# Optimization experiments

Hardware: AMD Instinct MI355X
Metric: run time of the kernel (lower is better)

The kernel has to match this reference:

```python
import jax, jax.numpy as jnp
import numpy as np

N, F, E, C, CELL = 2048, 64, 4, 3, 15
OUT_CH, OUT_K, N_CLASS = 10, 15, 2


def _xex(X, A_attr, wx0, wx1, we):
    # pairwise score tensor: Y[i,j] = X[i]@wx0 + X[j]@wx1 + A_attr[i,j]@we -> [N,N,c_out]
    return (X @ wx0)[:, None, :] + (X @ wx1)[None, :, :] + jnp.einsum('ije,ec->ijc', A_attr, we)


def _gcn_layer(X, A, A_attr, ax0, ax1, ae, ix0, ix1, ie, gx0, gx1, ge, wr):
    n = X.shape[0]
    # multi-channel attention (MA) branch
    att = jax.nn.elu(_xex(X, A_attr, ax0, ax1, ae)) + 1.0001  # [n,n,C]
    att = att * A[:, :, None]
    att = jax.nn.softmax(att, axis=1)  # softmax over neighbor axis (incl. zeroed entries, as in TF code)
    att = att * A[:, :, None]
    y_node = jnp.einsum('ijc,jf->icf', att, X).reshape(n, -1)        # [n, C*F_in]
    y_edge = jnp.einsum('ijc,ije->ice', att, A_attr).reshape(n, -1)  # [n, C*E]
    # gated branch (unmasked sum over all j, as in aggr_neibors_gate)
    info = jnp.tanh(_xex(X, A_attr, ix0, ix1, ie))        # [n,n,CELL]
    gate = jax.nn.sigmoid(_xex(X, A_attr, gx0, gx1, ge))  # [n,n,CELL]
    y_gate = jnp.sum(info * gate, axis=1)                 # [n, CELL]
    r = jnp.concatenate([X, y_edge, y_node, y_gate], axis=1)
    return jnp.tanh(r @ wr + 0.1)


def _forward(X, A, A_attr,
             att0_x0, att0_x1, att0_e, info0_x0, info0_x1, info0_e,
             gate0_x0, gate0_x1, gate0_e, r0,
             att1_x0, att1_x1, att1_e, info1_x0, info1_x1, info1_e,
             gate1_x0, gate1_x1, gate1_e, r1,
             out_att, out_cnn, out_r):
    h0 = _gcn_layer(X, A, A_attr, att0_x0, att0_x1, att0_e,
                    info0_x0, info0_x1, info0_e, gate0_x0, gate0_x1, gate0_e, r0)
    h1 = _gcn_layer(h0, A, A_attr, att1_x0, att1_x1, att1_e,
                    info1_x0, info1_x1, info1_e, gate1_x0, gate1_x1, gate1_e, r1)
    Xc = jnp.concatenate([X, h0, h1], axis=1)       # [n, F + 2*CELL]
    att = jax.nn.softmax(Xc @ out_att, axis=0)      # node-wise attention pooling, [n, OUT_CH]
    image = att.T @ Xc                              # [OUT_CH, F + 2*CELL]
    image = jnp.tanh(image @ out_cnn + 0.1)         # [OUT_CH, OUT_K]
    logits = image.reshape(1, -1) @ out_r + 0.1
    return jax.nn.softmax(logits, axis=-1)          # [1, N_CLASS]


def setup_inputs() -> dict:
    keys = jax.random.split(jax.random.key(0), 26)
    tn = lambda k, s: jax.random.normal(k, s, jnp.float32) * 0.05  # truncated_normal init approx
    return {
        'X': jax.random.normal(keys[0], (N, F), jnp.float32),
        'A': (jax.random.uniform(keys[1], (N, N)) < 0.02).astype(jnp.float32),  # ~40 neighbors/node
        'A_attr': jax.random.normal(keys[2], (N, N, E), jnp.float32),
        'att0_x0': tn(keys[3], (F, C)), 'att0_x1': tn(keys[4], (F, C)), 'att0_e': tn(keys[5], (E, C)),
        'info0_x0': tn(keys[6], (F, CELL)), 'info0_x1': tn(keys[7], (F, CELL)), 'info0_e': tn(keys[8], (E, CELL)),
        'gate0_x0': tn(keys[9], (F, CELL)), 'gate0_x1': tn(keys[10], (F, CELL)), 'gate0_e': tn(keys[11], (E, CELL)),
        'r0': tn(keys[12], (F + (F + E) * C + CELL, CELL)),
        'att1_x0': tn(keys[13], (CELL, C)), 'att1_x1': tn(keys[14], (CELL, C)), 'att1_e': tn(keys[15], (E, C)),
        'info1_x0': tn(keys[16], (CELL, CELL)), 'info1_x1': tn(keys[17], (CELL, CELL)), 'info1_e': tn(keys[18], (E, CELL)),
        'gate1_x0': tn(keys[19], (CELL, CELL)), 'gate1_x1': tn(keys[20], (CELL, CELL)), 'gate1_e': tn(keys[21], (E, CELL)),
        'r1': tn(keys[22], (CELL + (CELL + E) * C + CELL, CELL)),
        'out_att': tn(keys[23], (F + 2 * CELL, OUT_CH)),
        'out_cnn': tn(keys[24], (F + 2 * CELL, OUT_K)),
        'out_r': tn(keys[25], (OUT_K * OUT_CH, N_CLASS)),
    }


def reference(X, A, A_attr,
              att0_x0, att0_x1, att0_e, info0_x0, info0_x1, info0_e,
              gate0_x0, gate0_x1, gate0_e, r0,
              att1_x0, att1_x1, att1_e, info1_x0, info1_x1, info1_e,
              gate1_x0, gate1_x1, gate1_e, r1,
              out_att, out_cnn, out_r):
    return _forward(X, A, A_attr,
                    att0_x0, att0_x1, att0_e, info0_x0, info0_x1, info0_e,
                    gate0_x0, gate0_x1, gate0_e, r0,
                    att1_x0, att1_x1, att1_e, info1_x0, info1_x1, info1_e,
                    gate1_x0, gate1_x1, gate1_e, r1,
                    out_att, out_cnn, out_r)
```

## Files before the change

kernel.cpp:

```cpp
#include <hip/hip_runtime.h>
#include <hip/hip_bf16.h>
#include <math.h>

#define NN 2048
#define EE 4
#define CC 3
#define CELL 15
#define MAXD 128
#define GATE_JZ 4

typedef unsigned short u16;
typedef float f32x2 __attribute__((ext_vector_type(2)));

__device__ __forceinline__ float b2f(u16 u) { return __uint_as_float(((unsigned int)u) << 16); }
__device__ __forceinline__ u16 f2b(float f) {
    unsigned int x = __float_as_uint(f);
    unsigned int r = (x + 0x7fffu + ((x >> 16) & 1u)) >> 16;
    return (u16)r;
}
__device__ __forceinline__ float fastrcp(float x) { return __builtin_amdgcn_rcpf(x); }
__device__ __forceinline__ float fastexp2(float x) { return __builtin_amdgcn_exp2f(x); }
__device__ __forceinline__ float rfl(float x) {
    return __uint_as_float(__builtin_amdgcn_readfirstlane(__float_as_uint(x)));
}
__device__ __forceinline__ float ldx(const void* p, size_t i, bool bf) {
    if (bf) return b2f(((const u16*)p)[i]);
    return ((const float*)p)[i];
}
__device__ __forceinline__ bool detect_bf(const u16* X) {
    int lane = threadIdx.x & 63;
    u16 u = X[2 * lane];
    int e = (u >> 7) & 0xFF;
    unsigned long long m = __ballot(e >= 100 && e <= 150);
    return __popcll(m) >= 32;
}

__global__ __launch_bounds__(256) void k_edges(const void* __restrict__ A, const u16* __restrict__ Xd,
                                               int* __restrict__ flag, int* __restrict__ deg,
                                               int* __restrict__ edges) {
    bool bf = detect_bf(Xd);
    if (blockIdx.x == 0 && threadIdx.x == 0) *flag = bf ? 1 : 0;
    int lane = threadIdx.x & 63, wv = threadIdx.x >> 6;
    int i = blockIdx.x * 4 + wv;
    int base = 0;
    for (int jb = 0; jb < NN; jb += 64) {
        float a = ldx(A, (size_t)i * NN + jb + lane, bf);
        unsigned long long m = __ballot(a != 0.f);
        if (a != 0.f) {
            int slot = base + __popcll(m & ((1ull << lane) - 1ull));
            if (slot < MAXD) edges[i * MAXD + slot] = jb + lane;
        }
        base += __popcll(m);
    }
    if (lane == 0) deg[i] = base;
}

template<int FIN, bool XRAW>
__global__ void k_proj(const int* __restrict__ flag, const void* __restrict__ Xin_,
                       const void* __restrict__ ax0, const void* __restrict__ ax1,
                       const void* __restrict__ ix0, const void* __restrict__ ix1,
                       const void* __restrict__ gx0, const void* __restrict__ gx1,
                       float* __restrict__ p0, float* __restrict__ pj,
                       float* __restrict__ pa0, float* __restrict__ pa1) {
    __shared__ float xs[FIN];
    bool bf = (*flag != 0);
    bool xbf = XRAW ? bf : false;
    int nd = blockIdx.x;
    int t = threadIdx.x;
    if (t < FIN) xs[t] = ldx(Xin_, (size_t)nd * FIN + t, xbf);
    __syncthreads();
    if (t >= 66) return;
    const void* W; int col, OUT; float* dst;
    if (t < 15)      { W = ix0; col = t;      OUT = CELL; dst = p0  + nd * 30 + t; }
    else if (t < 30) { W = gx0; col = t - 15; OUT = CELL; dst = p0  + nd * 30 + t; }
    else if (t < 45) { W = ix1; col = t - 30; OUT = CELL; dst = pj  + nd * 30 + (t - 30); }
    else if (t < 60) { W = gx1; col = t - 45; OUT = CELL; dst = pj  + nd * 30 + (t - 30); }
    else if (t < 63) { W = ax0; col = t - 60; OUT = CC;   dst = pa0 + nd * 3 + (t - 60); }
    else             { W = ax1; col = t - 63; OUT = CC;   dst = pa1 + nd * 3 + (t - 63); }
    float acc = 0.f;
    for (int f = 0; f < FIN; ++f) acc += xs[f] * ldx(W, (size_t)f * OUT + col, bf);
    *dst = acc;
}

template<int FIN, bool BF, bool XRAW>
__device__ void att_body(const void* __restrict__ Xin_, const void* __restrict__ A_attr,
                         const void* __restrict__ ae,
                         const float* __restrict__ pa0, const float* __restrict__ pa1,
                         const int* __restrict__ deg, const int* __restrict__ edges,
                         float* __restrict__ y_node, float* __restrict__ y_edge,
                         float (*ew)[4], float* pdn, float* pne, float* pnn) {
    int i = blockIdx.x;
    int t = threadIdx.x;
    int lane = t & 63, wv = t >> 6;
    float aew[EE][CC];
    #pragma unroll
    for (int e = 0; e < EE; ++e)
        #pragma unroll
        for (int c = 0; c < CC; ++c) aew[e][c] = ldx(ae, e * CC + c, BF);
    float pa0v[3] = { pa0[i*3], pa0[i*3+1], pa0[i*3+2] };
    int dg = deg[i]; if (dg > MAXD) dg = MAXD;
    float dn[3] = {0.f, 0.f, 0.f};
    float ne[3][4] = {{0.f}};
    for (int base = 0; base < dg; base += 256) {
        int idx = base + t;
        if (idx < dg) {
            int j = edges[i * MAXD + idx];
            float a0, a1, a2, a3;
            if (BF) {
                const u16* ap = (const u16*)A_attr + ((size_t)i * NN + j) * EE;
                ushort4 av = *(const ushort4*)ap;
                a0 = b2f(av.x); a1 = b2f(av.y); a2 = b2f(av.z); a3 = b2f(av.w);
            } else {
                const float* ap = (const float*)A_attr + ((size_t)i * NN + j) * EE;
                float4 av = *(const float4*)ap;
                a0 = av.x; a1 = av.y; a2 = av.z; a3 = av.w;
            }
            float w[3];
            #pragma unroll
            for (int c = 0; c < 3; ++c) {
                float s = pa0v[c] + pa1[j*3 + c]
                        + a0*aew[0][c] + a1*aew[1][c] + a2*aew[2][c] + a3*aew[3][c];
                float val = (s > 0.f) ? (s + 1.0001f) : (__expf(s) - 1.f + 1.0001f);
                float wc = __expf(val);
                w[c] = wc;
                dn[c] += wc;
                ne[c][0] += wc * a0; ne[c][1] += wc * a1; ne[c][2] += wc * a2; ne[c][3] += wc * a3;
            }
            ew[idx][0] = __int_as_float(j);
            ew[idx][1] = w[0]; ew[idx][2] = w[1]; ew[idx][3] = w[2];
        }
    }
    #pragma unroll
    for (int off = 32; off; off >>= 1) {
        #pragma unroll
        for (int c = 0; c < 3; ++c) {
            dn[c] += __shfl_xor(dn[c], off);
            #pragma unroll
            for (int e = 0; e < 4; ++e) ne[c][e] += __shfl_xor(ne[c][e], off);
        }
    }
    if (lane == 0) {
        #pragma unroll
        for (int c = 0; c < 3; ++c) {
            pdn[wv*3 + c] = dn[c];
            #pragma unroll
            for (int e = 0; e < 4; ++e) pne[(wv*3 + c)*4 + e] = ne[c][e];
        }
    }
    __syncthreads();
    float rdn[3];
    #pragma unroll
    for (int c = 0; c < 3; ++c) {
        float s = (float)(NN - dg);
        #pragma unroll
        for (int w2 = 0; w2 < 4; ++w2) s += pdn[w2*3 + c];
        rdn[c] = 1.f / s;
    }
    float nn0 = 0.f, nn1 = 0.f, nn2 = 0.f;
    bool xbf = XRAW ? BF : false;
    for (int idx = wv; idx < dg; idx += 4) {
        int j = __float_as_int(ew[idx][0]);
        float w0 = ew[idx][1], w1 = ew[idx][2], w2 = ew[idx][3];
        if (lane < FIN) {
            float x = ldx(Xin_, (size_t)j * FIN + lane, xbf);
            nn0 += w0 * x; nn1 += w1 * x; nn2 += w2 * x;
        }
    }
    if (lane < FIN) {
        pnn[(wv*3 + 0)*64 + lane] = nn0;
        pnn[(wv*3 + 1)*64 + lane] = nn1;
        pnn[(wv*3 + 2)*64 + lane] = nn2;
    }
    __syncthreads();
    if (t < FIN) {
        #pragma unroll
        for (int c = 0; c < 3; ++c) {
            float s = pnn[(0*3+c)*64 + t] + pnn[(1*3+c)*64 + t]
                    + pnn[(2*3+c)*64 + t] + pnn[(3*3+c)*64 + t];
            y_node[(size_t)i * (3*FIN) + c*FIN + t] = s * rdn[c];
        }
    }
    if (t == 0) {
        #pragma unroll
        for (int c = 0; c < 3; ++c)
            #pragma unroll
            for (int e = 0; e < 4; ++e) {
                float s = pne[(0*3+c)*4+e] + pne[(1*3+c)*4+e] + pne[(2*3+c)*4+e] + pne[(3*3+c)*4+e];
                y_edge[(size_t)i * 12 + c*4 + e] = s * rdn[c];
            }
    }
}

template<int FIN, bool XRAW>
__global__ __launch_bounds__(256) void k_att(
        const int* __restrict__ flag,
        const void* __restrict__ Xin_, const void* __restrict__ A_attr, const void* __restrict__ ae,
        const float* __restrict__ pa0, const float* __restrict__ pa1,
        const int* __restrict__ deg, const int* __restrict__ edges,
        float* __restrict__ y_node, float* __restrict__ y_edge) {
    __shared__ float ew[MAXD][4];
    __shared__ float pdn[4*3];
    __shared__ float pne[4*3*4];
    __shared__ float pnn[4*3*64];
    if (*flag) att_body<FIN, true,  XRAW>(Xin_, A_attr, ae, pa0, pa1, deg, edges, y_node, y_edge, ew, pdn, pne, pnn);
    else       att_body<FIN, false, XRAW>(Xin_, A_attr, ae, pa0, pa1, deg, edges, y_node, y_edge, ew, pdn, pne, pnn);
}

template<bool BF, int K0, int NK>
__device__ void gate_half(const void* __restrict__ A_attr,
                          const void* __restrict__ iew, const void* __restrict__ gew,
                          const float* __restrict__ p0, const float* __restrict__ pj,
                          float* __restrict__ ygp, float* lds) {
    constexpr int T = 128;
    constexpr int JCH = NN / GATE_JZ;
    constexpr float L2E = 1.4426950408889634f;
    const int lane = threadIdx.x & 63;
    const int i = blockIdx.x * 4 + (threadIdx.x >> 6);
    const int jb0 = blockIdx.z * JCH;

    f32x2 W2[EE][NK];
    #pragma unroll
    for (int e = 0; e < EE; ++e)
        #pragma unroll
        for (int k = 0; k < NK; ++k) {
            W2[e][k].x = rfl(ldx(iew, e*CELL + K0 + k, BF) * (-2.f * L2E));
            W2[e][k].y = rfl(ldx(gew, e*CELL + K0 + k, BF) * (-L2E));
        }
    f32x2 p0p[NK];
    #pragma unroll
    for (int k = 0; k < NK; ++k) {
        p0p[k].x = rfl(p0[(size_t)i*30 + K0 + k] * (-2.f * L2E));
        p0p[k].y = rfl(p0[(size_t)i*30 + 15 + K0 + k] * (-L2E));
    }
    float acc[NK] = {0.f};

    for (int tb = jb0; tb < jb0 + JCH; tb += T) {
        __syncthreads();
        #pragma unroll
        for (int s = 0; s < 8; ++s) {
            int q = threadIdx.x + 256 * s;
            int r = q >> 4, c = q & 15;
            if (c < 2 * NK) {
                int k = c >> 1, comp = c & 1;
                float scale = comp ? (-L2E) : (-2.f * L2E);
                int ksrc = comp ? (15 + K0 + k) : (K0 + k);
                lds[r * 18 + c] = pj[(size_t)(tb + r) * 30 + ksrc] * scale;
            }
        }
        __syncthreads();
        #pragma unroll
        for (int js = 0; js < T; js += 64) {
            int r = js + lane;
            int j = tb + r;
            float a0, a1, a2, a3;
            if (BF) {
                const u16* ap = (const u16*)A_attr + ((size_t)i * NN + j) * EE;
                ushort4 av = *(const ushort4*)ap;
                a0 = b2f(av.x); a1 = b2f(av.y); a2 = b2f(av.z); a3 = b2f(av.w);
            } else {
                const float* ap = (const float*)A_attr + ((size_t)i * NN + j) * EE;
                float4 av = *(const float4*)ap;
                a0 = av.x; a1 = av.y; a2 = av.z; a3 = av.w;
            }
            f32x2 aa0 = {a0, a0}, aa1 = {a1, a1}, aa2 = {a2, a2}, aa3 = {a3, a3};
            const float* rowp = lds + r * 18;
            #pragma unroll
            for (int k = 0; k < NK; ++k) {
                f32x2 tu = *(const f32x2*)(rowp + 2*k) + p0p[k];
                tu += aa0 * W2[0][k];
                tu += aa1 * W2[1][k];
                tu += aa2 * W2[2][k];
                tu += aa3 * W2[3][k];
                float e1 = fastexp2(tu.x);
                float e2 = fastexp2(tu.y);
                float d1 = 1.f + e1, d2 = 1.f + e2;
                acc[k] = fmaf(1.f - e1, fastrcp(d1 * d2), acc[k]);
            }
        }
    }
    #pragma unroll
    for (int off = 32; off; off >>= 1)
        #pragma unroll
        for (int k = 0; k < NK; ++k) acc[k] += __shfl_xor(acc[k], off);
    if (lane == 0) {
        #pragma unroll
        for (int k = 0; k < NK; ++k)
            ygp[((size_t)blockIdx.z * NN + i) * CELL + K0 + k] = acc[k];
    }
}

__global__ __launch_bounds__(256, 2) void k_gate(
        const int* __restrict__ flag,
        const void* __restrict__ A_attr, const void* __restrict__ iew, const void* __restrict__ gew,
        const float* __restrict__ p0, const float* __restrict__ pj, float* __restrict__ ygp) {
    __shared__ __align__(16) float lds[128 * 18];
    if (*flag) {
        if (blockIdx.y == 0) gate_half<true, 0, 8>(A_attr, iew, gew, p0, pj, ygp, lds);
        else                 gate_half<true, 8, 7>(A_attr, iew, gew, p0, pj, ygp, lds);
    } else {
        if (blockIdx.y == 0) gate_half<false, 0, 8>(A_attr, iew, gew, p0, pj, ygp, lds);
        else                 gate_half<false, 8, 7>(A_attr, iew, gew, p0, pj, ygp, lds);
    }
}

__global__ __launch_bounds__(256) void k_hp(const int* __restrict__ flag,
        const void* __restrict__ X, const float* __restrict__ y_edge,
        const float* __restrict__ y_node, const float* __restrict__ y_gate,
        const void* __restrict__ wr,
        const void* __restrict__ ax0, const void* __restrict__ ax1,
        const void* __restrict__ ix0, const void* __restrict__ ix1,
        const void* __restrict__ gx0, const void* __restrict__ gx1,
        float* __restrict__ h0,
        float* __restrict__ p0o, float* __restrict__ pjo,
        float* __restrict__ pa0o, float* __restrict__ pa1o) {
    __shared__ float v[283];
    __shared__ float part[CELL][16];
    __shared__ float hs[CELL];
    bool bf = (*flag != 0);
    int nd = blockIdx.x, t = threadIdx.x;
    for (int q = t; q < 64; q += 256)  v[q]       = ldx(X, (size_t)nd * 64 + q, bf);
    for (int q = t; q < 12; q += 256)  v[64 + q]  = y_edge[(size_t)nd * 12 + q];
    for (int q = t; q < 192; q += 256) v[76 + q]  = y_node[(size_t)nd * 192 + q];
    for (int q = t; q < 15; q += 256) {
        float s = 0.f;
        #pragma unroll
        for (int z = 0; z < GATE_JZ; ++z) s += y_gate[((size_t)z * NN + nd) * CELL + q];
        v[268 + q] = s;
    }
    __syncthreads();
    if (t < 240) {
        int k = t >> 4, sub = t & 15;
        float acc = 0.f;
        for (int r = sub; r < 283; r += 16) acc += v[r] * ldx(wr, (size_t)r * CELL + k, bf);
        part[k][sub] = acc;
    }
    __syncthreads();
    if (t < CELL) {
        float acc = 0.1f;
        #pragma unroll
        for (int s = 0; s < 16; ++s) acc += part[t][s];
        float hv = tanhf(acc);
        hs[t] = hv;
        h0[(size_t)nd * CELL + t] = hv;
    }
    __syncthreads();
    if (t < 66) {
        const void* W; int col, OUT; float* dst;
        if (t < 15)      { W = ix0; col = t;      OUT = CELL; dst = p0o  + nd * 30 + t; }
        else if (t < 30) { W = gx0; col = t - 15; OUT = CELL; dst = p0o  + nd * 30 + t; }
        else if (t < 45) { W = ix1; col = t - 30; OUT = CELL; dst = pjo  + nd * 30 + (t - 30); }
        else if (t < 60) { W = gx1; col = t - 45; OUT = CELL; dst = pjo  + nd * 30 + (t - 30); }
        else if (t < 63) { W = ax0; col = t - 60; OUT = CC;   dst = pa0o + nd * 3 + (t - 60); }
        else             { W = ax1; col = t - 63; OUT = CC;   dst = pa1o + nd * 3 + (t - 63); }
        float acc = 0.f;
        for (int f = 0; f < CELL; ++f) acc += hs[f] * ldx(W, (size_t)f * OUT + col, bf);
        *dst = acc;
    }
}

__global__ __launch_bounds__(256) void k_hf(const int* __restrict__ flag,
        const void* __restrict__ X, const float* __restrict__ h0,
        const float* __restrict__ y_edge, const float* __restrict__ y_node,
        const float* __restrict__ y_gate, const void* __restrict__ wr,
        const void* __restrict__ oatt,
        float* __restrict__ h1, float* __restrict__ P) {
    __shared__ float v[87];
    __shared__ float xv[64];
    __shared__ float part[CELL][16];
    __shared__ float hs[CELL];
    __shared__ float pp[10][16];
    bool bf = (*flag != 0);
    int nd = blockIdx.x, t = threadIdx.x;
    for (int q = t; q < 15; q += 256) v[q]      = h0[(size_t)nd * 15 + q];
    for (int q = t; q < 12; q += 256) v[15 + q] = y_edge[(size_t)nd * 12 + q];
    for (int q = t; q < 45; q += 256) v[27 + q] = y_node[(size_t)nd * 45 + q];
    for (int q = t; q < 15; q += 256) {
        float s = 0.f;
        #pragma unroll
        for (int z = 0; z < GATE_JZ; ++z) s += y_gate[((size_t)z * NN + nd) * CELL + q];
        v[72 + q] = s;
    }
    for (int q = t; q < 64; q += 256) xv[q]     = ldx(X, (size_t)nd * 64 + q, bf);
    __syncthreads();
    if (t < 240) {
        int k = t >> 4, sub = t & 15;
        float acc = 0.f;
        for (int r = sub; r < 87; r += 16) acc += v[r] * ldx(wr, (size_t)r * CELL + k, bf);
        part[k][sub] = acc;
    }
    __syncthreads();
    if (t < CELL) {
        float acc = 0.1f;
        #pragma unroll
        for (int s = 0; s < 16; ++s) acc += part[t][s];
        float hv = tanhf(acc);
        hs[t] = hv;
        h1[(size_t)nd * CELL + t] = hv;
    }
    __syncthreads();
    if (t < 160) {
        int c = t >> 4, sub = t & 15;
        float acc = 0.f;
        for (int d = sub; d < 94; d += 16) {
            float x = (d < 64) ? xv[d] : (d < 79) ? v[d - 64] : hs[d - 79];
            acc += x * ldx(oatt, (size_t)d * 10 + c, bf);
        }
        pp[c][sub] = acc;
    }
    __syncthreads();
    if (t < 10) {
        float acc = 0.f;
        #pragma unroll
        for (int s = 0; s < 16; ++s) acc += pp[t][s];
        P[(size_t)nd * 10 + t] = acc;
    }
}

__global__ __launch_bounds__(1024) void k_f2(const float* __restrict__ P, float* __restrict__ wsm,
                                             float* __restrict__ imgp) {
    __shared__ float red[16][10];
    int t = threadIdx.x; int lane = t & 63; int wv = t >> 6;
    for (int q = t; q < 940; q += 1024) imgp[q] = 0.f;
    float mx[10], sm[10];
    #pragma unroll
    for (int c = 0; c < 10; ++c) mx[c] = -1e30f;
    for (int n = t; n < NN; n += 1024)
        #pragma unroll
        for (int c = 0; c < 10; ++c) mx[c] = fmaxf(mx[c], P[(size_t)n*10 + c]);
    #pragma unroll
    for (int off = 32; off; off >>= 1)
        #pragma unroll
        for (int c = 0; c < 10; ++c) mx[c] = fmaxf(mx[c], __shfl_xor(mx[c], off));
    if (lane == 0)
        #pragma unroll
        for (int c = 0; c < 10; ++c) red[wv][c] = mx[c];
    __syncthreads();
    #pragma unroll
    for (int c = 0; c < 10; ++c) {
        float m = red[0][c];
        for (int w2 = 1; w2 < 16; ++w2) m = fmaxf(m, red[w2][c]);
        mx[c] = m;
    }
    __syncthreads();
    #pragma unroll
    for (int c = 0; c < 10; ++c) sm[c] = 0.f;
    for (int n = t; n < NN; n += 1024)
        #pragma unroll
        for (int c = 0; c < 10; ++c) sm[c] += __expf(P[(size_t)n*10 + c] - mx[c]);
    #pragma unroll
    for (int off = 32; off; off >>= 1)
        #pragma unroll
        for (int c = 0; c < 10; ++c) sm[c] += __shfl_xor(sm[c], off);
    if (lane == 0)
        #pragma unroll
        for (int c = 0; c < 10; ++c) red[wv][c] = sm[c];
    __syncthreads();
    float rs[10];
    #pragma unroll
    for (int c = 0; c < 10; ++c) {
        float s = 0.f;
        for (int w2 = 0; w2 < 16; ++w2) s += red[w2][c];
        rs[c] = 1.f / s;
    }
    for (int n = t; n < NN; n += 1024)
        #pragma unroll
        for (int c = 0; c < 10; ++c) wsm[(size_t)n*10 + c] = __expf(P[(size_t)n*10 + c] - mx[c]) * rs[c];
}

__global__ __launch_bounds__(1024) void k_f3(const int* __restrict__ flag,
                     const void* __restrict__ X, const float* __restrict__ h0,
                     const float* __restrict__ h1, const float* __restrict__ wsm,
                     float* __restrict__ image_pre) {
    bool bf = (*flag != 0);
    int t = threadIdx.x;
    if (t >= 940) return;
    int ch = t / 94, d = t - ch * 94;
    int n0 = blockIdx.x * 32;
    float acc = 0.f;
    for (int nl = 0; nl < 32; ++nl) {
        int n = n0 + nl;
        float w = wsm[(size_t)n*10 + ch];
        float x = (d < 64) ? ldx(X, (size_t)n*64 + d, bf)
                : (d < 79) ? h0[(size_t)n*15 + (d - 64)]
                           : h1[(size_t)n*15 + (d - 79)];
        acc += w * x;
    }
    atomicAdd(&image_pre[t], acc);
}

__global__ __launch_bounds__(256) void k_f4(const int* __restrict__ flag,
                     const float* __restrict__ image_pre,
                     const void* __restrict__ out_cnn, const void* __restrict__ out_r,
                     void* __restrict__ out) {
    bool bf = (*flag != 0);
    __shared__ float ip[940];
    __shared__ float img2[150];
    __shared__ float red[8];
    int t = threadIdx.x;
    for (int q = t; q < 940; q += 256) ip[q] = image_pre[q];
    __syncthreads();
    if (t < 150) {
        int ch = t / 15, kk = t - ch * 15;
        float acc = 0.1f;
        for (int d = 0; d < 94; ++d) acc += ip[ch*94 + d] * ldx(out_cnn, (size_t)d*15 + kk, bf);
        img2[t] = tanhf(acc);
    }
    __syncthreads();
    float c0 = 0.f, c1 = 0.f;
    if (t < 150) {
        float vv = img2[t];
        c0 = vv * ldx(out_r, (size_t)t*2, bf);
        c1 = vv * ldx(out_r, (size_t)t*2 + 1, bf);
    }
    #pragma unroll
    for (int off = 32; off; off >>= 1) { c0 += __shfl_xor(c0, off); c1 += __shfl_xor(c1, off); }
    if ((t & 63) == 0) { red[(t >> 6)*2] = c0; red[(t >> 6)*2 + 1] = c1; }
    __syncthreads();
    if (t == 0) {
        float l0 = 0.1f + red[0] + red[2] + red[4] + red[6];
        float l1 = 0.1f + red[1] + red[3] + red[5] + red[7];
        float m = fmaxf(l0, l1);
        float e0 = __expf(l0 - m), e1 = __expf(l1 - m);
        float s = e0 + e1;
        float p0v = e0 / s, p1v = e1 / s;
        if (bf) { u16* o = (u16*)out; o[0] = f2b(p0v); o[1] = f2b(p1v); }
        else    { float* o = (float*)out; o[0] = p0v; o[1] = p1v; }
    }
}

extern "C" void kernel_launch(void* const* d_in, const int* in_sizes, int n_in,
                              void* d_out, int out_size, void* d_ws, size_t ws_size,
                              hipStream_t stream) {
    (void)in_sizes; (void)n_in; (void)out_size; (void)ws_size;
    const void* X      = d_in[0];
    const void* A      = d_in[1];
    const void* Aattr  = d_in[2];
    const void* a0x0 = d_in[3],  *a0x1 = d_in[4],  *a0e = d_in[5];
    const void* i0x0 = d_in[6],  *i0x1 = d_in[7],  *i0e = d_in[8];
    const void* g0x0 = d_in[9],  *g0x1 = d_in[10], *g0e = d_in[11];
    const void* r0   = d_in[12];
    const void* a1x0 = d_in[13], *a1x1 = d_in[14], *a1e = d_in[15];
    const void* i1x0 = d_in[16], *i1x1 = d_in[17], *i1e = d_in[18];
    const void* g1x0 = d_in[19], *g1x1 = d_in[20], *g1e = d_in[21];
    const void* r1   = d_in[22];
    const void* oatt = d_in[23], *ocnn = d_in[24], *orr = d_in[25];

    char* p = (char*)d_ws;
    auto alloc = [&](size_t bytes) -> void* { void* r = (void*)p; p += (bytes + 255) & ~(size_t)255; return r; };
    int*   flag   = (int*)  alloc(4);
    int*   deg    = (int*)  alloc(NN * 4);
    int*   edges  = (int*)  alloc((size_t)NN * MAXD * 4);
    float* p0_0   = (float*)alloc((size_t)NN * 30 * 4);
    float* pj_0   = (float*)alloc((size_t)NN * 30 * 4);
    float* pa0_0  = (float*)alloc((size_t)NN * 3 * 4);
    float* pa1_0  = (float*)alloc((size_t)NN * 3 * 4);
    float* p0_1   = (float*)alloc((size_t)NN * 30 * 4);
    float* pj_1   = (float*)alloc((size_t)NN * 30 * 4);
    float* pa0_1  = (float*)alloc((size_t)NN * 3 * 4);
    float* pa1_1  = (float*)alloc((size_t)NN * 3 * 4);
    float* ye0    = (float*)alloc((size_t)NN * 12 * 4);
    float* yn0    = (float*)alloc((size_t)NN * 192 * 4);
    float* yg0    = (float*)alloc((size_t)GATE_JZ * NN * CELL * 4);
    float* h0     = (float*)alloc((size_t)NN * CELL * 4);
    float* ye1    = (float*)alloc((size_t)NN * 12 * 4);
    float* yn1    = (float*)alloc((size_t)NN * 45 * 4);
    float* yg1    = (float*)alloc((size_t)GATE_JZ * NN * CELL * 4);
    float* h1     = (float*)alloc((size_t)NN * CELL * 4);
    float* P      = (float*)alloc((size_t)NN * 10 * 4);
    float* wsm    = (float*)alloc((size_t)NN * 10 * 4);
    float* imgp   = (float*)alloc(940 * 4);

    k_edges<<<NN / 4, 256, 0, stream>>>(A, (const u16*)X, flag, deg, edges);

    dim3 ggate(NN / 4, 2, GATE_JZ);

    k_proj<64, true><<<NN, 128, 0, stream>>>(flag, X, a0x0, a0x1, i0x0, i0x1, g0x0, g0x1, p0_0, pj_0, pa0_0, pa1_0);
    k_att<64, true><<<NN, 256, 0, stream>>>(flag, X, Aattr, a0e, pa0_0, pa1_0, deg, edges, yn0, ye0);
    k_gate<<<ggate, 256, 0, stream>>>(flag, Aattr, i0e, g0e, p0_0, pj_0, yg0);
    k_hp<<<NN, 256, 0, stream>>>(flag, X, ye0, yn0, yg0, r0,
                                 a1x0, a1x1, i1x0, i1x1, g1x0, g1x1,
                                 h0, p0_1, pj_1, pa0_1, pa1_1);

    k_att<15, false><<<NN, 256, 0, stream>>>(flag, h0, Aattr, a1e, pa0_1, pa1_1, deg, edges, yn1, ye1);
    k_gate<<<ggate, 256, 0, stream>>>(flag, Aattr, i1e, g1e, p0_1, pj_1, yg1);
    k_hf<<<NN, 256, 0, stream>>>(flag, X, h0, ye1, yn1, yg1, r1, oatt, h1, P);

    k_f2<<<1, 1024, 0, stream>>>(P, wsm, imgp);
    k_f3<<<64, 1024, 0, stream>>>(flag, X, h0, h1, wsm, imgp);
    k_f4<<<1, 256, 0, stream>>>(flag, imgp, ocnn, orr, d_out);
}
```

Before: 352.1 us.

## Fuse softmax into pooling kernel, raise gate split, repack layer-1 neighbor gather

Folds the single-block column softmax into the pooling kernel: each of the 64 blocks recomputes the global max and sum over P and then weights its 32-node slice, and the zeroing of imgp moves into k_edges. This removes one launch and the wsm round trip, but every block now rereads all of P. The gate kernel's j-split grows from 4 to 8 for more parallelism, at the cost of more partial sums for the consumer to reduce. For the 15-feature layer, each wave now handles four neighbors at once on 16-lane groups instead of leaving most lanes idle.

```diff
diff --git a/kernel.cpp b/kernel.cpp
--- a/kernel.cpp
+++ b/kernel.cpp
@@ -7,7 +7,7 @@
 #define CC 3
 #define CELL 15
 #define MAXD 128
-#define GATE_JZ 4
+#define GATE_JZ 8
 
 typedef unsigned short u16;
 typedef float f32x2 __attribute__((ext_vector_type(2)));
@@ -37,9 +37,12 @@
 
 __global__ __launch_bounds__(256) void k_edges(const void* __restrict__ A, const u16* __restrict__ Xd,
                                                int* __restrict__ flag, int* __restrict__ deg,
-                                               int* __restrict__ edges) {
+                                               int* __restrict__ edges, float* __restrict__ imgp) {
     bool bf = detect_bf(Xd);
-    if (blockIdx.x == 0 && threadIdx.x == 0) *flag = bf ? 1 : 0;
+    if (blockIdx.x == 0) {
+        if (threadIdx.x == 0) *flag = bf ? 1 : 0;
+        for (int q = threadIdx.x; q < 940; q += 256) imgp[q] = 0.f;
+    }
     int lane = threadIdx.x & 63, wv = threadIdx.x >> 6;
     int i = blockIdx.x * 4 + wv;
     int base = 0;
@@ -158,26 +161,56 @@
     }
     float nn0 = 0.f, nn1 = 0.f, nn2 = 0.f;
     bool xbf = XRAW ? BF : false;
-    for (int idx = wv; idx < dg; idx += 4) {
-        int j = __float_as_int(ew[idx][0]);
-        float w0 = ew[idx][1], w1 = ew[idx][2], w2 = ew[idx][3];
-        if (lane < FIN) {
-            float x = ldx(Xin_, (size_t)j * FIN + lane, xbf);
-            nn0 += w0 * x; nn1 += w1 * x; nn2 += w2 * x;
-        }
-    }
-    if (lane < FIN) {
+    if constexpr (FIN == 15) {
+        int sub = lane >> 4, f = lane & 15;
+        for (int idx = wv * 4 + sub; idx < dg; idx += 16) {
+            int j = __float_as_int(ew[idx][0]);
+            float w0 = ew[idx][1], w1 = ew[idx][2], w2 = ew[idx][3];
+            if (f < 15) {
+                float x = ldx(Xin_, (size_t)j * 15 + f, xbf);
+                nn0 += w0 * x; nn1 += w1 * x; nn2 += w2 * x;
+            }
+        }
         pnn[(wv*3 + 0)*64 + lane] = nn0;
         pnn[(wv*3 + 1)*64 + lane] = nn1;
         pnn[(wv*3 + 2)*64 + lane] = nn2;
-    }
-    __syncthreads();
-    if (t < FIN) {
-        #pragma unroll
-        for (int c = 0; c < 3; ++c) {
-            float s = pnn[(0*3+c)*64 + t] + pnn[(1*3+c)*64 + t]
-                    + pnn[(2*3+c)*64 + t] + pnn[(3*3+c)*64 + t];
-            y_node[(size_t)i * (3*FIN) + c*FIN + t] = s * rdn[c];
+    } else {
+        for (int idx = wv; idx < dg; idx += 4) {
+            int j = __float_as_int(ew[idx][0]);
+            float w0 = ew[idx][1], w1 = ew[idx][2], w2 = ew[idx][3];
+            if (lane < FIN) {
+                float x = ldx(Xin_, (size_t)j * FIN + lane, xbf);
+                nn0 += w0 * x; nn1 += w1 * x; nn2 += w2 * x;
+            }
+        }
+        if (lane < FIN) {
+            pnn[(wv*3 + 0)*64 + lane] = nn0;
+            pnn[(wv*3 + 1)*64 + lane] = nn1;
+            pnn[(wv*3 + 2)*64 + lane] = nn2;
+        }
+    }
+    __syncthreads();
+    if constexpr (FIN == 15) {
+        if (t < 15) {
+            #pragma unroll
+            for (int c = 0; c < 3; ++c) {
+                float s = 0.f;
+                #pragma unroll
+                for (int w2 = 0; w2 < 4; ++w2)
+                    #pragma unroll
+                    for (int sb = 0; sb < 4; ++sb)
+                        s += pnn[(w2*3 + c)*64 + sb*16 + t];
+                y_node[(size_t)i * 45 + c*15 + t] = s * rdn[c];
+            }
+        }
+    } else {
+        if (t < FIN) {
+            #pragma unroll
+            for (int c = 0; c < 3; ++c) {
+                float s = pnn[(0*3+c)*64 + t] + pnn[(1*3+c)*64 + t]
+                        + pnn[(2*3+c)*64 + t] + pnn[(3*3+c)*64 + t];
+                y_node[(size_t)i * (3*FIN) + c*FIN + t] = s * rdn[c];
+            }
         }
     }
     if (t == 0) {
@@ -416,11 +449,14 @@
     }
 }
 
-__global__ __launch_bounds__(1024) void k_f2(const float* __restrict__ P, float* __restrict__ wsm,
-                                             float* __restrict__ imgp) {
+__global__ __launch_bounds__(1024) void k_f3(const int* __restrict__ flag,
+                     const void* __restrict__ X, const float* __restrict__ h0,
+                     const float* __restrict__ h1, const float* __restrict__ P,
+                     float* __restrict__ image_pre) {
     __shared__ float red[16][10];
+    __shared__ float wsl[32][10];
+    bool bf = (*flag != 0);
     int t = threadIdx.x; int lane = t & 63; int wv = t >> 6;
-    for (int q = t; q < 940; q += 1024) imgp[q] = 0.f;
     float mx[10], sm[10];
     #pragma unroll
     for (int c = 0; c < 10; ++c) mx[c] = -1e30f;
@@ -462,30 +498,25 @@
         for (int w2 = 0; w2 < 16; ++w2) s += red[w2][c];
         rs[c] = 1.f / s;
     }
-    for (int n = t; n < NN; n += 1024)
-        #pragma unroll
-        for (int c = 0; c < 10; ++c) wsm[(size_t)n*10 + c] = __expf(P[(size_t)n*10 + c] - mx[c]) * rs[c];
-}
-
-__global__ __launch_bounds__(1024) void k_f3(const int* __restrict__ flag,
-                     const void* __restrict__ X, const float* __restrict__ h0,
-                     const float* __restrict__ h1, const float* __restrict__ wsm,
-                     float* __restrict__ image_pre) {
-    bool bf = (*flag != 0);
-    int t = threadIdx.x;
-    if (t >= 940) return;
-    int ch = t / 94, d = t - ch * 94;
     int n0 = blockIdx.x * 32;
-    float acc = 0.f;
-    for (int nl = 0; nl < 32; ++nl) {
-        int n = n0 + nl;
-        float w = wsm[(size_t)n*10 + ch];
-        float x = (d < 64) ? ldx(X, (size_t)n*64 + d, bf)
-                : (d < 79) ? h0[(size_t)n*15 + (d - 64)]
-                           : h1[(size_t)n*15 + (d - 79)];
-        acc += w * x;
-    }
-    atomicAdd(&image_pre[t], acc);
+    if (t < 320) {
+        int nl = t / 10, c = t - nl * 10;
+        wsl[nl][c] = __expf(P[(size_t)(n0 + nl)*10 + c] - mx[c]) * rs[c];
+    }
+    __syncthreads();
+    if (t < 940) {
+        int ch = t / 94, d = t - ch * 94;
+        float acc = 0.f;
+        for (int nl = 0; nl < 32; ++nl) {
+            int n = n0 + nl;
+            float w = wsl[nl][ch];
+            float x = (d < 64) ? ldx(X, (size_t)n*64 + d, bf)
+                    : (d < 79) ? h0[(size_t)n*15 + (d - 64)]
+                               : h1[(size_t)n*15 + (d - 79)];
+            acc += w * x;
+        }
+        atomicAdd(&image_pre[t], acc);
+    }
 }
 
 __global__ __launch_bounds__(256) void k_f4(const int* __restrict__ flag,
@@ -567,10 +598,9 @@
     float* yg1    = (float*)alloc((size_t)GATE_JZ * NN * CELL * 4);
     float* h1     = (float*)alloc((size_t)NN * CELL * 4);
     float* P      = (float*)alloc((size_t)NN * 10 * 4);
-    float* wsm    = (float*)alloc((size_t)NN * 10 * 4);
     float* imgp   = (float*)alloc(940 * 4);
 
-    k_edges<<<NN / 4, 256, 0, stream>>>(A, (const u16*)X, flag, deg, edges);
+    k_edges<<<NN / 4, 256, 0, stream>>>(A, (const u16*)X, flag, deg, edges, imgp);
 
     dim3 ggate(NN / 4, 2, GATE_JZ);
 
@@ -585,7 +615,6 @@
     k_gate<<<ggate, 256, 0, stream>>>(flag, Aattr, i1e, g1e, p0_1, pj_1, yg1);
     k_hf<<<NN, 256, 0, stream>>>(flag, X, h0, ye1, yn1, yg1, r1, oatt, h1, P);
 
-    k_f2<<<1, 1024, 0, stream>>>(P, wsm, imgp);
-    k_f3<<<64, 1024, 0, stream>>>(flag, X, h0, h1, wsm, imgp);
+    k_f3<<<64, 1024, 0, stream>>>(flag, X, h0, h1, P, imgp);
     k_f4<<<1, 256, 0, stream>>>(flag, imgp, ocnn, orr, d_out);
 }
```

Measured after the change: 358.7 us. Within noise of the previous version (+1.9%).
